# Kernel tuning notes

Hardware: AMD Instinct MI355X
Metric: run time of the kernel (lower is better)

The kernel has to match this reference:

```python
import jax, jax.numpy as jnp
import numpy as np

DIM = 32
BATCH = 131072
NH = 100

def _init_linear(key, nin, nout):
    k1, k2 = jax.random.split(key)
    bound = 1.0 / np.sqrt(nin)
    W = jax.random.uniform(k1, (nin, nout), minval=-bound, maxval=bound, dtype=jnp.float32)
    b = jax.random.uniform(k2, (nout,), minval=-bound, maxval=bound, dtype=jnp.float32)
    return W, b

def setup_inputs() -> dict:
    key = jax.random.key(0)
    ks = jax.random.split(key, 8)
    e = jax.random.normal(ks[0], (BATCH, DIM), dtype=jnp.float32)
    # causal adjacency: strictly upper-triangular random 0/1 (parents j of node i satisfy j < i)
    Craw = jax.random.bernoulli(ks[1], 0.5, (DIM, DIM)).astype(jnp.float32)
    C = Craw * jnp.triu(jnp.ones((DIM, DIM), jnp.float32), k=1)
    s_W1, s_b1 = _init_linear(ks[2], DIM, NH)
    s_W2, s_b2 = _init_linear(ks[3], NH, NH)
    s_W3, s_b3 = _init_linear(ks[4], NH, 1)
    t_W1, t_b1 = _init_linear(ks[5], DIM, NH)
    t_W2, t_b2 = _init_linear(ks[6], NH, NH)
    t_W3, t_b3 = _init_linear(ks[7], NH, 1)
    return {"e": e, "C": C,
            "s_W1": s_W1, "s_b1": s_b1, "s_W2": s_W2, "s_b2": s_b2, "s_W3": s_W3, "s_b3": s_b3,
            "t_W1": t_W1, "t_b1": t_b1, "t_W2": t_W2, "t_b2": t_b2, "t_W3": t_W3, "t_b3": t_b3}

def _mlp(x, W1, b1, W2, b2, W3, b3):
    # linear -> relu -> linear -> relu -> linear -> sigmoid, squeeze last dim
    h = jax.nn.relu(x @ W1 + b1)
    h = jax.nn.relu(h @ W2 + b2)
    return jax.nn.sigmoid(h @ W3 + b3)[:, 0]  # [B]

def reference(e, C, s_W1, s_b1, s_W2, s_b2, s_W3, s_b3, t_W1, t_b1, t_W2, t_b2, t_W3, t_b3):
    B, dim = e.shape

    def step(carry, xs):
        z, log_det = carry
        i, mask, e_i = xs          # mask = C[:, i] (all-zero column == zero mask branch in torch)
        x = z * mask               # [B, dim]
        s = _mlp(x, s_W1, s_b1, s_W2, s_b2, s_W3, s_b3)
        t = _mlp(x, t_W1, t_b1, t_W2, t_b2, t_W3, t_b3)
        z = z.at[:, i].set(jnp.exp(s) * e_i + t)
        return (z, log_det + s), None

    init = (jnp.zeros_like(e), jnp.zeros((B,), e.dtype))
    (z, log_det), _ = jax.lax.scan(step, init, (jnp.arange(dim), C.T, e.T))
    return z, log_det
```

## Files before the change

kernel.cpp:

```cpp
#include <hip/hip_runtime.h>


typedef __attribute__((ext_vector_type(8))) short short8;
typedef __attribute__((ext_vector_type(4))) float f32x4;
typedef __attribute__((ext_vector_type(4))) unsigned int uint4v;

#define WPK_U16 39936
#define MPK_OFF_BYTES 79872
#define NBLK 2048
#define REPS 4

__device__ __forceinline__ unsigned int bf16u(float v) {
  unsigned int b = __float_as_uint(v);
  b += 0x7FFFu + ((b >> 16) & 1u);
  return b >> 16;
}

__device__ __forceinline__ unsigned int cvtpk(float lo, float hi) {
  unsigned int r;
  asm("v_cvt_pk_bf16_f32 %0, %1, %2" : "=v"(r) : "v"(lo), "v"(hi));
  return r;
}

__device__ __forceinline__ unsigned int pkrelu(unsigned int x) {
  unsigned int r;
  asm("v_pk_max_i16 %0, %1, %2" : "=v"(r) : "v"(x), "v"(0u));
  return r;
}

__device__ __forceinline__ void pack_h(const f32x4 (&h)[7], uint4v (&B)[4],
                                       bool g1) {
#pragma unroll
  for (int c = 0; c < 3; ++c) {
    B[c].x = pkrelu(cvtpk(h[2 * c][0], h[2 * c][1]));
    B[c].y = pkrelu(cvtpk(h[2 * c][2], h[2 * c][3]));
    B[c].z = pkrelu(cvtpk(h[2 * c + 1][0], h[2 * c + 1][1]));
    B[c].w = pkrelu(cvtpk(h[2 * c + 1][2], h[2 * c + 1][3]));
  }
  float v0 = g1 ? 1.0f : h[6][0];
  B[3].x = pkrelu(cvtpk(v0, h[6][1]));
  B[3].y = pkrelu(cvtpk(h[6][2], h[6][3]));
  B[3].z = 0u;
  B[3].w = 0u;
}

__device__ __forceinline__ void mlp2_eval(
    const short8 (&a1s)[7], const short8 (&a2s)[7][4], const short8 (&a3s)[4],
    const short8 (&a1t)[7], const short8 (&a2t)[7][4], const short8 (&a3t)[4],
    short8 x, bool g1, float &sp, float &tp) {
  const f32x4 zz = {0.f, 0.f, 0.f, 0.f};
  f32x4 h1s[7], h1t[7];
#pragma unroll
  for (int t = 0; t < 7; ++t) {
    h1s[t] = __builtin_amdgcn_mfma_f32_16x16x32_bf16(a1s[t], x, zz, 0, 0, 0);
    h1t[t] = __builtin_amdgcn_mfma_f32_16x16x32_bf16(a1t[t], x, zz, 0, 0, 0);
  }
  uint4v B1s[4], B1t[4];
  pack_h(h1s, B1s, g1);
  pack_h(h1t, B1t, g1);
  f32x4 h2s[7], h2t[7];
#pragma unroll
  for (int t = 0; t < 7; ++t) { h2s[t] = zz; h2t[t] = zz; }
#pragma unroll
  for (int c = 0; c < 4; ++c) {
    short8 Bs = __builtin_bit_cast(short8, B1s[c]);
    short8 Bt = __builtin_bit_cast(short8, B1t[c]);
#pragma unroll
    for (int t = 0; t < 7; ++t) {
      h2s[t] = __builtin_amdgcn_mfma_f32_16x16x32_bf16(a2s[t][c], Bs, h2s[t], 0, 0, 0);
      h2t[t] = __builtin_amdgcn_mfma_f32_16x16x32_bf16(a2t[t][c], Bt, h2t[t], 0, 0, 0);
    }
  }
  uint4v B2s[4], B2t[4];
  pack_h(h2s, B2s, g1);
  pack_h(h2t, B2t, g1);
  f32x4 as0 = __builtin_amdgcn_mfma_f32_16x16x32_bf16(a3s[0], __builtin_bit_cast(short8, B2s[0]), zz, 0, 0, 0);
  f32x4 at0 = __builtin_amdgcn_mfma_f32_16x16x32_bf16(a3t[0], __builtin_bit_cast(short8, B2t[0]), zz, 0, 0, 0);
  f32x4 as1 = __builtin_amdgcn_mfma_f32_16x16x32_bf16(a3s[1], __builtin_bit_cast(short8, B2s[1]), zz, 0, 0, 0);
  f32x4 at1 = __builtin_amdgcn_mfma_f32_16x16x32_bf16(a3t[1], __builtin_bit_cast(short8, B2t[1]), zz, 0, 0, 0);
  f32x4 as2 = __builtin_amdgcn_mfma_f32_16x16x32_bf16(a3s[2], __builtin_bit_cast(short8, B2s[2]), zz, 0, 0, 0);
  f32x4 at2 = __builtin_amdgcn_mfma_f32_16x16x32_bf16(a3t[2], __builtin_bit_cast(short8, B2t[2]), zz, 0, 0, 0);
  f32x4 as3 = __builtin_amdgcn_mfma_f32_16x16x32_bf16(a3s[3], __builtin_bit_cast(short8, B2s[3]), zz, 0, 0, 0);
  f32x4 at3 = __builtin_amdgcn_mfma_f32_16x16x32_bf16(a3t[3], __builtin_bit_cast(short8, B2t[3]), zz, 0, 0, 0);
  sp = (as0[0] + as1[0]) + (as2[0] + as3[0]);
  tp = (at0[0] + at1[0]) + (at2[0] + at3[0]);
}

__global__ void prepack_kernel(const float *__restrict__ C,
                               const float *__restrict__ sW1, const float *__restrict__ sb1,
                               const float *__restrict__ sW2, const float *__restrict__ sb2,
                               const float *__restrict__ sW3, const float *__restrict__ sb3,
                               const float *__restrict__ tW1, const float *__restrict__ tb1,
                               const float *__restrict__ tW2, const float *__restrict__ tb2,
                               const float *__restrict__ tW3, const float *__restrict__ tb3,
                               unsigned short *__restrict__ wpk,
                               unsigned int *__restrict__ mpk) {
  int gid = blockIdx.x * 256 + threadIdx.x;
  if (gid < WPK_U16) {
    int which = gid / 19968;
    int a = gid % 19968;
    const float *W1 = which ? tW1 : sW1;
    const float *B1 = which ? tb1 : sb1;
    const float *W2 = which ? tW2 : sW2;
    const float *B2 = which ? tb2 : sb2;
    const float *W3 = which ? tW3 : sW3;
    const float *B3 = which ? tb3 : sb3;
    float v = 0.f;
    if (a < 3584) {
      int t = a >> 9; int rem = a & 511; int l = rem >> 3; int j = rem & 7;
      int m = 16 * t + (l & 15);
      int d = 8 * (l >> 4) + j;
      if (m < 100) {
        if (d == 31) v = B1[m];
        else v = W1[d * 100 + m];
      }
    } else if (a < 17920) {
      int b = a - 3584; int tc = b >> 9; int t = tc >> 2; int c = tc & 3;
      int rem = b & 511; int l = rem >> 3; int j = rem & 7;
      int m = 16 * t + (l & 15);
      int k = 32 * c + (j >> 2) * 16 + 4 * (l >> 4) + (j & 3);
      if (m < 100) {
        if (k < 100) v = W2[k * 100 + m];
        else if (k == 100) v = B2[m];
      }
    } else {
      int b = a - 17920; int c = b >> 9; int rem = b & 511;
      int l = rem >> 3; int j = rem & 7;
      int k = 32 * c + (j >> 2) * 16 + 4 * (l >> 4) + (j & 3);
      (void)l;
      if (k < 100) v = W3[k];
      else if (k == 100) v = B3[0];
    }
    wpk[gid] = (unsigned short)bf16u(v);
  } else if (gid < WPK_U16 + 512) {
    int idx = gid - WPK_U16;
    int i = idx >> 4;
    int G = (idx >> 2) & 3;
    int p = idx & 3;
    int d0 = 8 * G + 2 * p;
    unsigned int u = 0;
    if (C[d0 * 32 + i] != 0.f) u |= 0x0000FFFFu;
    if (C[(d0 + 1) * 32 + i] != 0.f) u |= 0xFFFF0000u;
    mpk[idx] = u;
  }
}

__global__ __launch_bounds__(64, 1) void flow_main(
    const float *__restrict__ e, const unsigned short *__restrict__ wpk,
    const unsigned int *__restrict__ mpk, float *__restrict__ out) {
  const int lane = threadIdx.x;
  const int G = lane >> 4;
  const int bl = lane & 15;
  const bool g1 = (G == 1);
  const bool g3 = (G == 3);

  __shared__ __align__(16) unsigned int msk[512];
  {
    const uint4v *s = (const uint4v *)mpk;
    uint4v *d = (uint4v *)msk;
    d[lane] = s[lane];
    d[lane + 64] = s[lane + 64];
  }

  const short8 *w = (const short8 *)wpk;
  short8 a1s[7], a2s[7][4], a3s[4];
  short8 a1t[7], a2t[7][4], a3t[4];
#pragma unroll
  for (int t = 0; t < 7; ++t) a1s[t] = w[t * 64 + lane];
#pragma unroll
  for (int t = 0; t < 7; ++t)
#pragma unroll
    for (int c = 0; c < 4; ++c) a2s[t][c] = w[448 + (t * 4 + c) * 64 + lane];
#pragma unroll
  for (int c = 0; c < 4; ++c) a3s[c] = w[2240 + c * 64 + lane];
#pragma unroll
  for (int t = 0; t < 7; ++t) a1t[t] = w[2496 + t * 64 + lane];
#pragma unroll
  for (int t = 0; t < 7; ++t)
#pragma unroll
    for (int c = 0; c < 4; ++c)
      a2t[t][c] = w[2496 + 448 + (t * 4 + c) * 64 + lane];
#pragma unroll
  for (int c = 0; c < 4; ++c) a3t[c] = w[2496 + 2240 + c * 64 + lane];

#pragma unroll 1
  for (int rep = 0; rep < REPS; ++rep) {
    const long base = ((long)blockIdx.x * REPS + rep) * 16;
    const float *ep = e + (base + bl) * 32 + G * 8;
    f32x4 e0 = *(const f32x4 *)ep;
    f32x4 e1 = *(const f32x4 *)(ep + 4);
    unsigned int z0 = 0, z1 = 0, z2 = 0, z3 = 0;
    float ld = 0.f;
    uint4v m = *(const uint4v *)&msk[G * 4];

#pragma unroll 1
    for (int i8 = 0; i8 < 4; ++i8) {
      const bool tg = (G == i8);
#pragma unroll
      for (int u = 0; u < 8; ++u) {
        const int i = i8 * 8 + u;
        uint4v mn = *(const uint4v *)&msk[((i + 1) & 31) * 16 + G * 4];
        unsigned int x0 = z0 & m.x, x1 = z1 & m.y, x2 = z2 & m.z, x3 = z3 & m.w;
        if (g3) x3 = (x3 & 0x0000FFFFu) | 0x3F800000u;
        uint4v xu; xu.x = x0; xu.y = x1; xu.z = x2; xu.w = x3;
        short8 x = __builtin_bit_cast(short8, xu);

        float sp, tp;
        mlp2_eval(a1s, a2s, a3s, a1t, a2t, a3t, x, g1, sp, tp);
        float sv = __fdividef(1.f, 1.f + __expf(-sp));
        float tv = __fdividef(1.f, 1.f + __expf(-tp));
        ld += sv;

        float es = (u < 4) ? e0[u] : e1[u - 4];
        float zn = __expf(sv) * es + tv;
        unsigned int r = cvtpk(zn, zn);
        const int p = (u >> 1) & 3;
        const bool hi = (u & 1) != 0;
        unsigned int mrg;
        if (p == 0) {
          mrg = hi ? ((z0 & 0x0000FFFFu) | (r & 0xFFFF0000u))
                   : ((z0 & 0xFFFF0000u) | (r & 0x0000FFFFu));
          z0 = tg ? mrg : z0;
        } else if (p == 1) {
          mrg = hi ? ((z1 & 0x0000FFFFu) | (r & 0xFFFF0000u))
                   : ((z1 & 0xFFFF0000u) | (r & 0x0000FFFFu));
          z1 = tg ? mrg : z1;
        } else if (p == 2) {
          mrg = hi ? ((z2 & 0x0000FFFFu) | (r & 0xFFFF0000u))
                   : ((z2 & 0xFFFF0000u) | (r & 0x0000FFFFu));
          z2 = tg ? mrg : z2;
        } else {
          mrg = hi ? ((z3 & 0x0000FFFFu) | (r & 0xFFFF0000u))
                   : ((z3 & 0xFFFF0000u) | (r & 0x0000FFFFu));
          z3 = tg ? mrg : z3;
        }
        m = mn;
      }
    }

    float *zo = out + (base + bl) * 32 + G * 8;
    f32x4 o0, o1;
    o0[0] = __uint_as_float(z0 << 16);
    o0[1] = __uint_as_float(z0 & 0xFFFF0000u);
    o0[2] = __uint_as_float(z1 << 16);
    o0[3] = __uint_as_float(z1 & 0xFFFF0000u);
    o1[0] = __uint_as_float(z2 << 16);
    o1[1] = __uint_as_float(z2 & 0xFFFF0000u);
    o1[2] = __uint_as_float(z3 << 16);
    o1[3] = __uint_as_float(z3 & 0xFFFF0000u);
    *(f32x4 *)zo = o0;
    *(f32x4 *)(zo + 4) = o1;
    if (lane < 16) out[(long)131072 * 32 + base + bl] = ld;
  }
}

extern "C" void kernel_launch(void *const *d_in, const int *in_sizes, int n_in,
                              void *d_out, int out_size, void *d_ws, size_t ws_size,
                              hipStream_t stream) {
  const float *e  = (const float *)d_in[0];
  const float *C  = (const float *)d_in[1];
  const float *sW1 = (const float *)d_in[2];
  const float *sb1 = (const float *)d_in[3];
  const float *sW2 = (const float *)d_in[4];
  const float *sb2 = (const float *)d_in[5];
  const float *sW3 = (const float *)d_in[6];
  const float *sb3 = (const float *)d_in[7];
  const float *tW1 = (const float *)d_in[8];
  const float *tb1 = (const float *)d_in[9];
  const float *tW2 = (const float *)d_in[10];
  const float *tb2 = (const float *)d_in[11];
  const float *tW3 = (const float *)d_in[12];
  const float *tb3 = (const float *)d_in[13];

  unsigned short *wpk = (unsigned short *)d_ws;
  unsigned int *mpk = (unsigned int *)((char *)d_ws + MPK_OFF_BYTES);
  float *out = (float *)d_out;

  prepack_kernel<<<dim3(159), dim3(256), 0, stream>>>(
      C, sW1, sb1, sW2, sb2, sW3, sb3, tW1, tb1, tW2, tb2, tW3, tb3, wpk, mpk);
  flow_main<<<dim3(NBLK), dim3(64), 0, stream>>>(e, wpk, mpk, out);
}
```

Measured before the change: 292.0 us.

## Switch MLP evaluation from 16x16x32 to 32x32x16 MFMA tiles

Restructures the per-step MLP so each wave handles 32 batch rows with 32x32x16 bf16 MFMAs instead of 16 rows with 16x16x32. Weight prepacking, mask packing and the z-state register layout are all redone for the new fragment shapes, and the grid is halved. The third-layer weights move to shared memory to ease register pressure. Larger tiles pad 100 up to 128 instead of 112, so more MFMA work is wasted, and layer-2 accumulation becomes longer serial chains.

```diff
diff --git a/kernel.cpp b/kernel.cpp
--- a/kernel.cpp
+++ b/kernel.cpp
@@ -3,11 +3,12 @@
 
 typedef __attribute__((ext_vector_type(8))) short short8;
 typedef __attribute__((ext_vector_type(4))) float f32x4;
+typedef __attribute__((ext_vector_type(16))) float f32x16;
 typedef __attribute__((ext_vector_type(4))) unsigned int uint4v;
 
-#define WPK_U16 39936
-#define MPK_OFF_BYTES 79872
-#define NBLK 2048
+#define WPK_U16 44032
+#define MPK_OFF_BYTES 88064
+#define NBLK 1024
 #define REPS 4
 
 __device__ __forceinline__ unsigned int bf16u(float v) {
@@ -28,62 +29,80 @@
   return r;
 }
 
-__device__ __forceinline__ void pack_h(const f32x4 (&h)[7], uint4v (&B)[4],
-                                       bool g1) {
-#pragma unroll
-  for (int c = 0; c < 3; ++c) {
-    B[c].x = pkrelu(cvtpk(h[2 * c][0], h[2 * c][1]));
-    B[c].y = pkrelu(cvtpk(h[2 * c][2], h[2 * c][3]));
-    B[c].z = pkrelu(cvtpk(h[2 * c + 1][0], h[2 * c + 1][1]));
-    B[c].w = pkrelu(cvtpk(h[2 * c + 1][2], h[2 * c + 1][3]));
-  }
-  float v0 = g1 ? 1.0f : h[6][0];
-  B[3].x = pkrelu(cvtpk(v0, h[6][1]));
-  B[3].y = pkrelu(cvtpk(h[6][2], h[6][3]));
-  B[3].z = 0u;
-  B[3].w = 0u;
-}
-
-__device__ __forceinline__ void mlp2_eval(
-    const short8 (&a1s)[7], const short8 (&a2s)[7][4], const short8 (&a3s)[4],
-    const short8 (&a1t)[7], const short8 (&a2t)[7][4], const short8 (&a3t)[4],
-    short8 x, bool g1, float &sp, float &tp) {
-  const f32x4 zz = {0.f, 0.f, 0.f, 0.f};
-  f32x4 h1s[7], h1t[7];
-#pragma unroll
-  for (int t = 0; t < 7; ++t) {
-    h1s[t] = __builtin_amdgcn_mfma_f32_16x16x32_bf16(a1s[t], x, zz, 0, 0, 0);
-    h1t[t] = __builtin_amdgcn_mfma_f32_16x16x32_bf16(a1t[t], x, zz, 0, 0, 0);
-  }
-  uint4v B1s[4], B1t[4];
-  pack_h(h1s, B1s, g1);
-  pack_h(h1t, B1t, g1);
-  f32x4 h2s[7], h2t[7];
-#pragma unroll
-  for (int t = 0; t < 7; ++t) { h2s[t] = zz; h2t[t] = zz; }
-#pragma unroll
-  for (int c = 0; c < 4; ++c) {
-    short8 Bs = __builtin_bit_cast(short8, B1s[c]);
-    short8 Bt = __builtin_bit_cast(short8, B1t[c]);
-#pragma unroll
-    for (int t = 0; t < 7; ++t) {
-      h2s[t] = __builtin_amdgcn_mfma_f32_16x16x32_bf16(a2s[t][c], Bs, h2s[t], 0, 0, 0);
-      h2t[t] = __builtin_amdgcn_mfma_f32_16x16x32_bf16(a2t[t][c], Bt, h2t[t], 0, 0, 0);
-    }
-  }
-  uint4v B2s[4], B2t[4];
-  pack_h(h2s, B2s, g1);
-  pack_h(h2t, B2t, g1);
-  f32x4 as0 = __builtin_amdgcn_mfma_f32_16x16x32_bf16(a3s[0], __builtin_bit_cast(short8, B2s[0]), zz, 0, 0, 0);
-  f32x4 at0 = __builtin_amdgcn_mfma_f32_16x16x32_bf16(a3t[0], __builtin_bit_cast(short8, B2t[0]), zz, 0, 0, 0);
-  f32x4 as1 = __builtin_amdgcn_mfma_f32_16x16x32_bf16(a3s[1], __builtin_bit_cast(short8, B2s[1]), zz, 0, 0, 0);
-  f32x4 at1 = __builtin_amdgcn_mfma_f32_16x16x32_bf16(a3t[1], __builtin_bit_cast(short8, B2t[1]), zz, 0, 0, 0);
-  f32x4 as2 = __builtin_amdgcn_mfma_f32_16x16x32_bf16(a3s[2], __builtin_bit_cast(short8, B2s[2]), zz, 0, 0, 0);
-  f32x4 at2 = __builtin_amdgcn_mfma_f32_16x16x32_bf16(a3t[2], __builtin_bit_cast(short8, B2t[2]), zz, 0, 0, 0);
-  f32x4 as3 = __builtin_amdgcn_mfma_f32_16x16x32_bf16(a3s[3], __builtin_bit_cast(short8, B2s[3]), zz, 0, 0, 0);
-  f32x4 at3 = __builtin_amdgcn_mfma_f32_16x16x32_bf16(a3t[3], __builtin_bit_cast(short8, B2t[3]), zz, 0, 0, 0);
-  sp = (as0[0] + as1[0]) + (as2[0] + as3[0]);
-  tp = (at0[0] + at1[0]) + (at2[0] + at3[0]);
+__device__ __forceinline__ short8 packBC(const f32x16 &ht, int c) {
+  uint4v u;
+  u.x = pkrelu(cvtpk(ht[c * 8 + 0], ht[c * 8 + 1]));
+  u.y = pkrelu(cvtpk(ht[c * 8 + 2], ht[c * 8 + 3]));
+  u.z = pkrelu(cvtpk(ht[c * 8 + 4], ht[c * 8 + 5]));
+  u.w = pkrelu(cvtpk(ht[c * 8 + 6], ht[c * 8 + 7]));
+  return __builtin_bit_cast(short8, u);
+}
+
+__device__ __forceinline__ short8 packBC6(const f32x16 &ht, bool bh) {
+  uint4v u;
+  float lo = bh ? 1.0f : ht[0];
+  u.x = pkrelu(cvtpk(lo, ht[1]));
+  u.y = pkrelu(cvtpk(ht[2], ht[3]));
+  u.z = pkrelu(cvtpk(ht[4], ht[5]));
+  u.w = pkrelu(cvtpk(ht[6], ht[7]));
+  return __builtin_bit_cast(short8, u);
+}
+
+__device__ __forceinline__ float mlp32(const short8 (&a1)[4][2],
+                                       const short8 (&a2)[4][7],
+                                       const short8 *__restrict__ a3,
+                                       short8 x0, short8 x1, bool bh) {
+  const f32x16 zz = {0.f, 0.f, 0.f, 0.f, 0.f, 0.f, 0.f, 0.f,
+                     0.f, 0.f, 0.f, 0.f, 0.f, 0.f, 0.f, 0.f};
+  f32x16 h1[4];
+#pragma unroll
+  for (int T = 0; T < 4; ++T)
+    h1[T] = __builtin_amdgcn_mfma_f32_32x32x16_bf16(a1[T][0], x0, zz, 0, 0, 0);
+#pragma unroll
+  for (int T = 0; T < 4; ++T)
+    h1[T] = __builtin_amdgcn_mfma_f32_32x32x16_bf16(a1[T][1], x1, h1[T], 0, 0, 0);
+
+  short8 bf0 = packBC(h1[0], 0), bf1 = packBC(h1[0], 1);
+  short8 bf2 = packBC(h1[1], 0), bf3 = packBC(h1[1], 1);
+  short8 bf4 = packBC(h1[2], 0), bf5 = packBC(h1[2], 1);
+  short8 bf6 = packBC6(h1[3], bh);
+
+  f32x16 h2[4];
+#pragma unroll
+  for (int M = 0; M < 4; ++M)
+    h2[M] = __builtin_amdgcn_mfma_f32_32x32x16_bf16(a2[M][0], bf0, zz, 0, 0, 0);
+#pragma unroll
+  for (int M = 0; M < 4; ++M)
+    h2[M] = __builtin_amdgcn_mfma_f32_32x32x16_bf16(a2[M][1], bf1, h2[M], 0, 0, 0);
+#pragma unroll
+  for (int M = 0; M < 4; ++M)
+    h2[M] = __builtin_amdgcn_mfma_f32_32x32x16_bf16(a2[M][2], bf2, h2[M], 0, 0, 0);
+#pragma unroll
+  for (int M = 0; M < 4; ++M)
+    h2[M] = __builtin_amdgcn_mfma_f32_32x32x16_bf16(a2[M][3], bf3, h2[M], 0, 0, 0);
+#pragma unroll
+  for (int M = 0; M < 4; ++M)
+    h2[M] = __builtin_amdgcn_mfma_f32_32x32x16_bf16(a2[M][4], bf4, h2[M], 0, 0, 0);
+#pragma unroll
+  for (int M = 0; M < 4; ++M)
+    h2[M] = __builtin_amdgcn_mfma_f32_32x32x16_bf16(a2[M][5], bf5, h2[M], 0, 0, 0);
+#pragma unroll
+  for (int M = 0; M < 4; ++M)
+    h2[M] = __builtin_amdgcn_mfma_f32_32x32x16_bf16(a2[M][6], bf6, h2[M], 0, 0, 0);
+
+  short8 bg0 = packBC(h2[0], 0), bg1 = packBC(h2[0], 1);
+  short8 bg2 = packBC(h2[1], 0), bg3 = packBC(h2[1], 1);
+  short8 bg4 = packBC(h2[2], 0), bg5 = packBC(h2[2], 1);
+  short8 bg6 = packBC6(h2[3], bh);
+
+  f32x16 acc0 = __builtin_amdgcn_mfma_f32_32x32x16_bf16(a3[0], bg0, zz, 0, 0, 0);
+  f32x16 acc1 = __builtin_amdgcn_mfma_f32_32x32x16_bf16(a3[64], bg1, zz, 0, 0, 0);
+  acc0 = __builtin_amdgcn_mfma_f32_32x32x16_bf16(a3[128], bg2, acc0, 0, 0, 0);
+  acc1 = __builtin_amdgcn_mfma_f32_32x32x16_bf16(a3[192], bg3, acc1, 0, 0, 0);
+  acc0 = __builtin_amdgcn_mfma_f32_32x32x16_bf16(a3[256], bg4, acc0, 0, 0, 0);
+  acc1 = __builtin_amdgcn_mfma_f32_32x32x16_bf16(a3[320], bg5, acc1, 0, 0, 0);
+  acc0 = __builtin_amdgcn_mfma_f32_32x32x16_bf16(a3[384], bg6, acc0, 0, 0, 0);
+  return acc0[0] + acc1[0];
 }
 
 __global__ void prepack_kernel(const float *__restrict__ C,
@@ -97,47 +116,48 @@
                                unsigned int *__restrict__ mpk) {
   int gid = blockIdx.x * 256 + threadIdx.x;
   if (gid < WPK_U16) {
-    int which = gid / 19968;
-    int a = gid % 19968;
+    int which = gid / 22016;
+    int a = gid % 22016;
     const float *W1 = which ? tW1 : sW1;
     const float *B1 = which ? tb1 : sb1;
     const float *W2 = which ? tW2 : sW2;
     const float *B2 = which ? tb2 : sb2;
     const float *W3 = which ? tW3 : sW3;
     const float *B3 = which ? tb3 : sb3;
+    int f = a >> 9;
+    int l = (a >> 3) & 63;
+    int j = a & 7;
+    int hh = l >> 5, cl = l & 31;
     float v = 0.f;
-    if (a < 3584) {
-      int t = a >> 9; int rem = a & 511; int l = rem >> 3; int j = rem & 7;
-      int m = 16 * t + (l & 15);
-      int d = 8 * (l >> 4) + j;
+    if (f < 8) {
+      int T = f >> 1, c = f & 1;
+      int m = 32 * T + cl;
+      int d = 16 * c + 8 * hh + j;
+      if (m < 100) v = (d == 31) ? B1[m] : W1[d * 100 + m];
+    } else if (f < 36) {
+      int ff = f - 8;
+      int M = ff / 7, kk = ff % 7;
+      int m = 32 * M + cl;
+      int q = (kk & 1) * 8 + j;
+      int n = 32 * (kk >> 1) + (q & 3) + 8 * (q >> 2) + 4 * hh;
       if (m < 100) {
-        if (d == 31) v = B1[m];
-        else v = W1[d * 100 + m];
-      }
-    } else if (a < 17920) {
-      int b = a - 3584; int tc = b >> 9; int t = tc >> 2; int c = tc & 3;
-      int rem = b & 511; int l = rem >> 3; int j = rem & 7;
-      int m = 16 * t + (l & 15);
-      int k = 32 * c + (j >> 2) * 16 + 4 * (l >> 4) + (j & 3);
-      if (m < 100) {
-        if (k < 100) v = W2[k * 100 + m];
-        else if (k == 100) v = B2[m];
+        if (n < 100) v = W2[n * 100 + m];
+        else if (n == 100) v = B2[m];
       }
     } else {
-      int b = a - 17920; int c = b >> 9; int rem = b & 511;
-      int l = rem >> 3; int j = rem & 7;
-      int k = 32 * c + (j >> 2) * 16 + 4 * (l >> 4) + (j & 3);
-      (void)l;
-      if (k < 100) v = W3[k];
-      else if (k == 100) v = B3[0];
+      int kk = f - 36;
+      int q = (kk & 1) * 8 + j;
+      int n = 32 * (kk >> 1) + (q & 3) + 8 * (q >> 2) + 4 * hh;
+      if (n < 100) v = W3[n];
+      else if (n == 100) v = B3[0];
     }
     wpk[gid] = (unsigned short)bf16u(v);
   } else if (gid < WPK_U16 + 512) {
     int idx = gid - WPK_U16;
     int i = idx >> 4;
-    int G = (idx >> 2) & 3;
-    int p = idx & 3;
-    int d0 = 8 * G + 2 * p;
+    int hh = (idx >> 3) & 1;
+    int p = idx & 7;
+    int d0 = 16 * (p >> 2) + 8 * hh + 2 * (p & 3);
     unsigned int u = 0;
     if (C[d0 * 32 + i] != 0.f) u |= 0x0000FFFFu;
     if (C[(d0 + 1) * 32 + i] != 0.f) u |= 0xFFFF0000u;
@@ -149,108 +169,126 @@
     const float *__restrict__ e, const unsigned short *__restrict__ wpk,
     const unsigned int *__restrict__ mpk, float *__restrict__ out) {
   const int lane = threadIdx.x;
-  const int G = lane >> 4;
-  const int bl = lane & 15;
-  const bool g1 = (G == 1);
-  const bool g3 = (G == 3);
+  const int h = lane >> 5;
+  const int col = lane & 31;
+  const bool hb = (h == 1);
 
   __shared__ __align__(16) unsigned int msk[512];
+  __shared__ short8 a3l[896];
   {
     const uint4v *s = (const uint4v *)mpk;
     uint4v *d = (uint4v *)msk;
     d[lane] = s[lane];
     d[lane + 64] = s[lane + 64];
   }
-
-  const short8 *w = (const short8 *)wpk;
-  short8 a1s[7], a2s[7][4], a3s[4];
-  short8 a1t[7], a2t[7][4], a3t[4];
-#pragma unroll
-  for (int t = 0; t < 7; ++t) a1s[t] = w[t * 64 + lane];
-#pragma unroll
-  for (int t = 0; t < 7; ++t)
-#pragma unroll
-    for (int c = 0; c < 4; ++c) a2s[t][c] = w[448 + (t * 4 + c) * 64 + lane];
-#pragma unroll
-  for (int c = 0; c < 4; ++c) a3s[c] = w[2240 + c * 64 + lane];
-#pragma unroll
-  for (int t = 0; t < 7; ++t) a1t[t] = w[2496 + t * 64 + lane];
-#pragma unroll
-  for (int t = 0; t < 7; ++t)
-#pragma unroll
-    for (int c = 0; c < 4; ++c)
-      a2t[t][c] = w[2496 + 448 + (t * 4 + c) * 64 + lane];
-#pragma unroll
-  for (int c = 0; c < 4; ++c) a3t[c] = w[2496 + 2240 + c * 64 + lane];
+  const short8 *wfr = (const short8 *)wpk;
+#pragma unroll
+  for (int f = 0; f < 14; ++f) {
+    int mlp = f / 7, kk = f % 7;
+    a3l[f * 64 + lane] = wfr[(mlp * 43 + 36 + kk) * 64 + lane];
+  }
+
+  short8 a1s[4][2], a2s[4][7], a1t[4][2], a2t[4][7];
+#pragma unroll
+  for (int T = 0; T < 4; ++T)
+#pragma unroll
+    for (int c = 0; c < 2; ++c) {
+      a1s[T][c] = wfr[(T * 2 + c) * 64 + lane];
+      a1t[T][c] = wfr[(43 + T * 2 + c) * 64 + lane];
+    }
+#pragma unroll
+  for (int M = 0; M < 4; ++M)
+#pragma unroll
+    for (int k = 0; k < 7; ++k) {
+      a2s[M][k] = wfr[(8 + M * 7 + k) * 64 + lane];
+      a2t[M][k] = wfr[(43 + 8 + M * 7 + k) * 64 + lane];
+    }
+  __syncthreads();
+
+  const short8 *a3s = a3l + lane;
+  const short8 *a3t = a3l + 7 * 64 + lane;
 
 #pragma unroll 1
   for (int rep = 0; rep < REPS; ++rep) {
-    const long base = ((long)blockIdx.x * REPS + rep) * 16;
-    const float *ep = e + (base + bl) * 32 + G * 8;
-    f32x4 e0 = *(const f32x4 *)ep;
-    f32x4 e1 = *(const f32x4 *)(ep + 4);
-    unsigned int z0 = 0, z1 = 0, z2 = 0, z3 = 0;
+    const long row = ((long)blockIdx.x * REPS + rep) * 32 + col;
+    const float *ep = e + row * 32;
+    f32x4 eA = *(const f32x4 *)(ep + 8 * h);
+    f32x4 eB = *(const f32x4 *)(ep + 8 * h + 4);
+    f32x4 eC = *(const f32x4 *)(ep + 16 + 8 * h);
+    f32x4 eD = *(const f32x4 *)(ep + 16 + 8 * h + 4);
+    unsigned int zr[8] = {0u, 0u, 0u, 0u, 0u, 0u, 0u, 0u};
     float ld = 0.f;
-    uint4v m = *(const uint4v *)&msk[G * 4];
+    uint4v ma = *(const uint4v *)&msk[h * 8];
+    uint4v mb = *(const uint4v *)&msk[h * 8 + 4];
 
 #pragma unroll 1
     for (int i8 = 0; i8 < 4; ++i8) {
-      const bool tg = (G == i8);
+      const bool tg = (h == (i8 & 1));
 #pragma unroll
       for (int u = 0; u < 8; ++u) {
-        const int i = i8 * 8 + u;
-        uint4v mn = *(const uint4v *)&msk[((i + 1) & 31) * 16 + G * 4];
-        unsigned int x0 = z0 & m.x, x1 = z1 & m.y, x2 = z2 & m.z, x3 = z3 & m.w;
-        if (g3) x3 = (x3 & 0x0000FFFFu) | 0x3F800000u;
-        uint4v xu; xu.x = x0; xu.y = x1; xu.z = x2; xu.w = x3;
-        short8 x = __builtin_bit_cast(short8, xu);
-
-        float sp, tp;
-        mlp2_eval(a1s, a2s, a3s, a1t, a2t, a3t, x, g1, sp, tp);
+        const int nx = (((i8 * 8 + u) + 1) & 31) * 16 + h * 8;
+        uint4v man = *(const uint4v *)&msk[nx];
+        uint4v mbn = *(const uint4v *)&msk[nx + 4];
+
+        uint4v xu0, xu1;
+        xu0.x = zr[0] & ma.x; xu0.y = zr[1] & ma.y;
+        xu0.z = zr[2] & ma.z; xu0.w = zr[3] & ma.w;
+        xu1.x = zr[4] & mb.x; xu1.y = zr[5] & mb.y;
+        xu1.z = zr[6] & mb.z; xu1.w = zr[7] & mb.w;
+        if (hb) xu1.w = (xu1.w & 0x0000FFFFu) | 0x3F800000u;
+        short8 x0 = __builtin_bit_cast(short8, xu0);
+        short8 x1 = __builtin_bit_cast(short8, xu1);
+
+        float sp = mlp32(a1s, a2s, a3s, x0, x1, hb);
+        float tp = mlp32(a1t, a2t, a3t, x0, x1, hb);
         float sv = __fdividef(1.f, 1.f + __expf(-sp));
         float tv = __fdividef(1.f, 1.f + __expf(-tp));
         ld += sv;
 
-        float es = (u < 4) ? e0[u] : e1[u - 4];
+        float es0 = (u < 4) ? eA[u] : eB[u - 4];
+        float es1 = (u < 4) ? eC[u] : eD[u - 4];
+        float es = (i8 < 2) ? es0 : es1;
         float zn = __expf(sv) * es + tv;
         unsigned int r = cvtpk(zn, zn);
-        const int p = (u >> 1) & 3;
+        const int p = u >> 1;
         const bool hi = (u & 1) != 0;
-        unsigned int mrg;
-        if (p == 0) {
-          mrg = hi ? ((z0 & 0x0000FFFFu) | (r & 0xFFFF0000u))
-                   : ((z0 & 0xFFFF0000u) | (r & 0x0000FFFFu));
-          z0 = tg ? mrg : z0;
-        } else if (p == 1) {
-          mrg = hi ? ((z1 & 0x0000FFFFu) | (r & 0xFFFF0000u))
-                   : ((z1 & 0xFFFF0000u) | (r & 0x0000FFFFu));
-          z1 = tg ? mrg : z1;
-        } else if (p == 2) {
-          mrg = hi ? ((z2 & 0x0000FFFFu) | (r & 0xFFFF0000u))
-                   : ((z2 & 0xFFFF0000u) | (r & 0x0000FFFFu));
-          z2 = tg ? mrg : z2;
+        if (i8 < 2) {
+          unsigned int mrg = hi ? ((zr[p] & 0x0000FFFFu) | (r & 0xFFFF0000u))
+                                : ((zr[p] & 0xFFFF0000u) | (r & 0x0000FFFFu));
+          zr[p] = tg ? mrg : zr[p];
         } else {
-          mrg = hi ? ((z3 & 0x0000FFFFu) | (r & 0xFFFF0000u))
-                   : ((z3 & 0xFFFF0000u) | (r & 0x0000FFFFu));
-          z3 = tg ? mrg : z3;
+          unsigned int mrg = hi ? ((zr[4 + p] & 0x0000FFFFu) | (r & 0xFFFF0000u))
+                                : ((zr[4 + p] & 0xFFFF0000u) | (r & 0x0000FFFFu));
+          zr[4 + p] = tg ? mrg : zr[4 + p];
         }
-        m = mn;
+        ma = man;
+        mb = mbn;
       }
     }
 
-    float *zo = out + (base + bl) * 32 + G * 8;
-    f32x4 o0, o1;
-    o0[0] = __uint_as_float(z0 << 16);
-    o0[1] = __uint_as_float(z0 & 0xFFFF0000u);
-    o0[2] = __uint_as_float(z1 << 16);
-    o0[3] = __uint_as_float(z1 & 0xFFFF0000u);
-    o1[0] = __uint_as_float(z2 << 16);
-    o1[1] = __uint_as_float(z2 & 0xFFFF0000u);
-    o1[2] = __uint_as_float(z3 << 16);
-    o1[3] = __uint_as_float(z3 & 0xFFFF0000u);
-    *(f32x4 *)zo = o0;
-    *(f32x4 *)(zo + 4) = o1;
-    if (lane < 16) out[(long)131072 * 32 + base + bl] = ld;
+    float *zo = out + row * 32;
+    f32x4 o;
+    o[0] = __uint_as_float(zr[0] << 16);
+    o[1] = __uint_as_float(zr[0] & 0xFFFF0000u);
+    o[2] = __uint_as_float(zr[1] << 16);
+    o[3] = __uint_as_float(zr[1] & 0xFFFF0000u);
+    *(f32x4 *)(zo + 8 * h) = o;
+    o[0] = __uint_as_float(zr[2] << 16);
+    o[1] = __uint_as_float(zr[2] & 0xFFFF0000u);
+    o[2] = __uint_as_float(zr[3] << 16);
+    o[3] = __uint_as_float(zr[3] & 0xFFFF0000u);
+    *(f32x4 *)(zo + 8 * h + 4) = o;
+    o[0] = __uint_as_float(zr[4] << 16);
+    o[1] = __uint_as_float(zr[4] & 0xFFFF0000u);
+    o[2] = __uint_as_float(zr[5] << 16);
+    o[3] = __uint_as_float(zr[5] & 0xFFFF0000u);
+    *(f32x4 *)(zo + 16 + 8 * h) = o;
+    o[0] = __uint_as_float(zr[6] << 16);
+    o[1] = __uint_as_float(zr[6] & 0xFFFF0000u);
+    o[2] = __uint_as_float(zr[7] << 16);
+    o[3] = __uint_as_float(zr[7] & 0xFFFF0000u);
+    *(f32x4 *)(zo + 16 + 8 * h + 4) = o;
+    if (h == 0) out[(long)131072 * 32 + row] = ld;
   }
 }
 
@@ -276,7 +314,7 @@
   unsigned int *mpk = (unsigned int *)((char *)d_ws + MPK_OFF_BYTES);
   float *out = (float *)d_out;
 
-  prepack_kernel<<<dim3(159), dim3(256), 0, stream>>>(
+  prepack_kernel<<<dim3(174), dim3(256), 0, stream>>>(
       C, sW1, sb1, sW2, sb2, sW3, sb3, tW1, tb1, tW2, tb2, tW3, tb3, wpk, mpk);
   flow_main<<<dim3(NBLK), dim3(64), 0, stream>>>(e, wpk, mpk, out);
 }
```

Result: faster. 282.3 us (-3.3%).

## Split s and t MLPs across two wavefronts with LDS exchange per step

Applied to the files above, without the earlier changes.

Each block now runs two waves. One evaluates the s-network and the other the t-network, each holding only its own weights in registers, with the layer-2 weights pinned to AGPRs. After every one of the 32 sequential steps the sigmoid outputs are swapped through shared memory using two barriers, so both waves can update the same z state. This halves per-wave MFMA work and register pressure and allows two blocks per CU. The cost is two __syncthreads per step on the serial critical path, plus a per-step global load of e instead of preloaded registers.

```diff
diff --git a/kernel.cpp b/kernel.cpp
--- a/kernel.cpp
+++ b/kernel.cpp
@@ -44,46 +44,34 @@
   B[3].w = 0u;
 }
 
-__device__ __forceinline__ void mlp2_eval(
-    const short8 (&a1s)[7], const short8 (&a2s)[7][4], const short8 (&a3s)[4],
-    const short8 (&a1t)[7], const short8 (&a2t)[7][4], const short8 (&a3t)[4],
-    short8 x, bool g1, float &sp, float &tp) {
+__device__ __forceinline__ float mlp_eval(const short8 (&a1)[7],
+                                          const short8 (&a2)[7][4],
+                                          const short8 (&a3)[4],
+                                          short8 x, bool g1) {
   const f32x4 zz = {0.f, 0.f, 0.f, 0.f};
-  f32x4 h1s[7], h1t[7];
-#pragma unroll
-  for (int t = 0; t < 7; ++t) {
-    h1s[t] = __builtin_amdgcn_mfma_f32_16x16x32_bf16(a1s[t], x, zz, 0, 0, 0);
-    h1t[t] = __builtin_amdgcn_mfma_f32_16x16x32_bf16(a1t[t], x, zz, 0, 0, 0);
-  }
-  uint4v B1s[4], B1t[4];
-  pack_h(h1s, B1s, g1);
-  pack_h(h1t, B1t, g1);
-  f32x4 h2s[7], h2t[7];
-#pragma unroll
-  for (int t = 0; t < 7; ++t) { h2s[t] = zz; h2t[t] = zz; }
+  f32x4 h1[7];
+#pragma unroll
+  for (int t = 0; t < 7; ++t)
+    h1[t] = __builtin_amdgcn_mfma_f32_16x16x32_bf16(a1[t], x, zz, 0, 0, 0);
+  uint4v B1[4];
+  pack_h(h1, B1, g1);
+  f32x4 h2[7];
+#pragma unroll
+  for (int t = 0; t < 7; ++t) h2[t] = zz;
 #pragma unroll
   for (int c = 0; c < 4; ++c) {
-    short8 Bs = __builtin_bit_cast(short8, B1s[c]);
-    short8 Bt = __builtin_bit_cast(short8, B1t[c]);
-#pragma unroll
-    for (int t = 0; t < 7; ++t) {
-      h2s[t] = __builtin_amdgcn_mfma_f32_16x16x32_bf16(a2s[t][c], Bs, h2s[t], 0, 0, 0);
-      h2t[t] = __builtin_amdgcn_mfma_f32_16x16x32_bf16(a2t[t][c], Bt, h2t[t], 0, 0, 0);
-    }
-  }
-  uint4v B2s[4], B2t[4];
-  pack_h(h2s, B2s, g1);
-  pack_h(h2t, B2t, g1);
-  f32x4 as0 = __builtin_amdgcn_mfma_f32_16x16x32_bf16(a3s[0], __builtin_bit_cast(short8, B2s[0]), zz, 0, 0, 0);
-  f32x4 at0 = __builtin_amdgcn_mfma_f32_16x16x32_bf16(a3t[0], __builtin_bit_cast(short8, B2t[0]), zz, 0, 0, 0);
-  f32x4 as1 = __builtin_amdgcn_mfma_f32_16x16x32_bf16(a3s[1], __builtin_bit_cast(short8, B2s[1]), zz, 0, 0, 0);
-  f32x4 at1 = __builtin_amdgcn_mfma_f32_16x16x32_bf16(a3t[1], __builtin_bit_cast(short8, B2t[1]), zz, 0, 0, 0);
-  f32x4 as2 = __builtin_amdgcn_mfma_f32_16x16x32_bf16(a3s[2], __builtin_bit_cast(short8, B2s[2]), zz, 0, 0, 0);
-  f32x4 at2 = __builtin_amdgcn_mfma_f32_16x16x32_bf16(a3t[2], __builtin_bit_cast(short8, B2t[2]), zz, 0, 0, 0);
-  f32x4 as3 = __builtin_amdgcn_mfma_f32_16x16x32_bf16(a3s[3], __builtin_bit_cast(short8, B2s[3]), zz, 0, 0, 0);
-  f32x4 at3 = __builtin_amdgcn_mfma_f32_16x16x32_bf16(a3t[3], __builtin_bit_cast(short8, B2t[3]), zz, 0, 0, 0);
-  sp = (as0[0] + as1[0]) + (as2[0] + as3[0]);
-  tp = (at0[0] + at1[0]) + (at2[0] + at3[0]);
+    short8 B = __builtin_bit_cast(short8, B1[c]);
+#pragma unroll
+    for (int t = 0; t < 7; ++t)
+      h2[t] = __builtin_amdgcn_mfma_f32_16x16x32_bf16(a2[t][c], B, h2[t], 0, 0, 0);
+  }
+  uint4v B2[4];
+  pack_h(h2, B2, g1);
+  f32x4 a0 = __builtin_amdgcn_mfma_f32_16x16x32_bf16(a3[0], __builtin_bit_cast(short8, B2[0]), zz, 0, 0, 0);
+  f32x4 a1r = __builtin_amdgcn_mfma_f32_16x16x32_bf16(a3[1], __builtin_bit_cast(short8, B2[1]), zz, 0, 0, 0);
+  f32x4 a2r = __builtin_amdgcn_mfma_f32_16x16x32_bf16(a3[2], __builtin_bit_cast(short8, B2[2]), zz, 0, 0, 0);
+  f32x4 a3r = __builtin_amdgcn_mfma_f32_16x16x32_bf16(a3[3], __builtin_bit_cast(short8, B2[3]), zz, 0, 0, 0);
+  return (a0[0] + a1r[0]) + (a2r[0] + a3r[0]);
 }
 
 __global__ void prepack_kernel(const float *__restrict__ C,
@@ -145,53 +133,46 @@
   }
 }
 
-__global__ __launch_bounds__(64, 1) void flow_main(
+__global__ __launch_bounds__(128, 2) void flow_main(
     const float *__restrict__ e, const unsigned short *__restrict__ wpk,
     const unsigned int *__restrict__ mpk, float *__restrict__ out) {
-  const int lane = threadIdx.x;
+  const int tid = threadIdx.x;
+  const int role = tid >> 6;
+  const int lane = tid & 63;
   const int G = lane >> 4;
   const int bl = lane & 15;
   const bool g1 = (G == 1);
   const bool g3 = (G == 3);
 
-  __shared__ __align__(16) unsigned int msk[512];
-  {
-    const uint4v *s = (const uint4v *)mpk;
-    uint4v *d = (uint4v *)msk;
-    d[lane] = s[lane];
-    d[lane + 64] = s[lane + 64];
-  }
-
-  const short8 *w = (const short8 *)wpk;
-  short8 a1s[7], a2s[7][4], a3s[4];
-  short8 a1t[7], a2t[7][4], a3t[4];
-#pragma unroll
-  for (int t = 0; t < 7; ++t) a1s[t] = w[t * 64 + lane];
+  __shared__ __align__(16) unsigned int shm[544];
+  volatile float *exf = (volatile float *)(shm + 512);
+  ((uint4v *)shm)[tid] = ((const uint4v *)mpk)[tid & 127];
+  if (tid < 32) exf[tid] = 0.f;
+
+  const short8 *w = (const short8 *)wpk + (role ? 2496 : 0);
+  short8 a1[7], a2[7][4], a3[4];
+#pragma unroll
+  for (int t = 0; t < 7; ++t) a1[t] = w[t * 64 + lane];
 #pragma unroll
   for (int t = 0; t < 7; ++t)
 #pragma unroll
-    for (int c = 0; c < 4; ++c) a2s[t][c] = w[448 + (t * 4 + c) * 64 + lane];
-#pragma unroll
-  for (int c = 0; c < 4; ++c) a3s[c] = w[2240 + c * 64 + lane];
-#pragma unroll
-  for (int t = 0; t < 7; ++t) a1t[t] = w[2496 + t * 64 + lane];
+    for (int c = 0; c < 4; ++c) a2[t][c] = w[448 + (t * 4 + c) * 64 + lane];
+#pragma unroll
+  for (int c = 0; c < 4; ++c) a3[c] = w[2240 + c * 64 + lane];
 #pragma unroll
   for (int t = 0; t < 7; ++t)
 #pragma unroll
-    for (int c = 0; c < 4; ++c)
-      a2t[t][c] = w[2496 + 448 + (t * 4 + c) * 64 + lane];
-#pragma unroll
-  for (int c = 0; c < 4; ++c) a3t[c] = w[2496 + 2240 + c * 64 + lane];
+    for (int c = 0; c < 4; ++c) asm volatile("" : "+a"(a2[t][c]));
+  __syncthreads();
 
 #pragma unroll 1
   for (int rep = 0; rep < REPS; ++rep) {
     const long base = ((long)blockIdx.x * REPS + rep) * 16;
-    const float *ep = e + (base + bl) * 32 + G * 8;
-    f32x4 e0 = *(const f32x4 *)ep;
-    f32x4 e1 = *(const f32x4 *)(ep + 4);
+    const long row = base + bl;
+    const float *erow = e + row * 32;
     unsigned int z0 = 0, z1 = 0, z2 = 0, z3 = 0;
     float ld = 0.f;
-    uint4v m = *(const uint4v *)&msk[G * 4];
+    uint4v m = *(const uint4v *)&shm[G * 4];
 
 #pragma unroll 1
     for (int i8 = 0; i8 < 4; ++i8) {
@@ -199,19 +180,24 @@
 #pragma unroll
       for (int u = 0; u < 8; ++u) {
         const int i = i8 * 8 + u;
-        uint4v mn = *(const uint4v *)&msk[((i + 1) & 31) * 16 + G * 4];
+        float es = erow[i];
+        uint4v mn = *(const uint4v *)&shm[((i + 1) & 31) * 16 + G * 4];
         unsigned int x0 = z0 & m.x, x1 = z1 & m.y, x2 = z2 & m.z, x3 = z3 & m.w;
         if (g3) x3 = (x3 & 0x0000FFFFu) | 0x3F800000u;
         uint4v xu; xu.x = x0; xu.y = x1; xu.z = x2; xu.w = x3;
         short8 x = __builtin_bit_cast(short8, xu);
 
-        float sp, tp;
-        mlp2_eval(a1s, a2s, a3s, a1t, a2t, a3t, x, g1, sp, tp);
-        float sv = __fdividef(1.f, 1.f + __expf(-sp));
-        float tv = __fdividef(1.f, 1.f + __expf(-tp));
+        float pval = mlp_eval(a1, a2, a3, x, g1);
+        float v = __fdividef(1.f, 1.f + __expf(-pval));
+
+        exf[role * 16 + bl] = v;
+        __syncthreads();
+        float other = exf[(role ^ 1) * 16 + bl];
+        __syncthreads();
+        float sv = role ? other : v;
+        float tv = role ? v : other;
         ld += sv;
 
-        float es = (u < 4) ? e0[u] : e1[u - 4];
         float zn = __expf(sv) * es + tv;
         unsigned int r = cvtpk(zn, zn);
         const int p = (u >> 1) & 3;
@@ -238,19 +224,21 @@
       }
     }
 
-    float *zo = out + (base + bl) * 32 + G * 8;
-    f32x4 o0, o1;
-    o0[0] = __uint_as_float(z0 << 16);
-    o0[1] = __uint_as_float(z0 & 0xFFFF0000u);
-    o0[2] = __uint_as_float(z1 << 16);
-    o0[3] = __uint_as_float(z1 & 0xFFFF0000u);
-    o1[0] = __uint_as_float(z2 << 16);
-    o1[1] = __uint_as_float(z2 & 0xFFFF0000u);
-    o1[2] = __uint_as_float(z3 << 16);
-    o1[3] = __uint_as_float(z3 & 0xFFFF0000u);
-    *(f32x4 *)zo = o0;
-    *(f32x4 *)(zo + 4) = o1;
-    if (lane < 16) out[(long)131072 * 32 + base + bl] = ld;
+    if (role == 0) {
+      float *zo = out + row * 32 + G * 8;
+      f32x4 o0, o1;
+      o0[0] = __uint_as_float(z0 << 16);
+      o0[1] = __uint_as_float(z0 & 0xFFFF0000u);
+      o0[2] = __uint_as_float(z1 << 16);
+      o0[3] = __uint_as_float(z1 & 0xFFFF0000u);
+      o1[0] = __uint_as_float(z2 << 16);
+      o1[1] = __uint_as_float(z2 & 0xFFFF0000u);
+      o1[2] = __uint_as_float(z3 << 16);
+      o1[3] = __uint_as_float(z3 & 0xFFFF0000u);
+      *(f32x4 *)zo = o0;
+      *(f32x4 *)(zo + 4) = o1;
+      if (lane < 16) out[(long)131072 * 32 + base + lane] = ld;
+    }
   }
 }
 
@@ -278,5 +266,5 @@
 
   prepack_kernel<<<dim3(159), dim3(256), 0, stream>>>(
       C, sW1, sb1, sW2, sb2, sW3, sb3, tW1, tb1, tW2, tb2, tW3, tb3, wpk, mpk);
-  flow_main<<<dim3(NBLK), dim3(64), 0, stream>>>(e, wpk, mpk, out);
-}
+  flow_main<<<dim3(NBLK), dim3(128), 0, stream>>>(e, wpk, mpk, out);
+}
```

Result: slower. 321.1 us (+10.0%).
